# Kernel optimization log

Measured on AMD Instinct MI355X. Metric: run time of the kernel, lower is better.

## Reference

```python
import jax, jax.numpy as jnp
import numpy as np

KSIZE = 7
NSPIX = 196


def _unfold(x, k):
    # x: (T, C, H, W) -> (T, C, k*k, H, W), reflect padding, torch Unfold ordering
    p = (k - 1) // 2
    T, C, H, W = x.shape
    xp = jnp.pad(x, ((0, 0), (0, 0), (p, p), (p, p)), mode='reflect')
    return jnp.stack([xp[:, :, i:i + H, j:j + W] for i in range(k) for j in range(k)], axis=2)


def setup_inputs() -> dict:
    key = jax.random.key(0)
    k1, k2, k3, k4, k5 = jax.random.split(key, 5)
    T, C, H, W = 2, 64, 160, 160
    fan_in = C * KSIZE * KSIZE
    x = jax.random.normal(k1, (T, C, H, W), jnp.float32)
    spix = jax.random.randint(k2, (T, H, W), 0, NSPIX, jnp.int32)
    W_lin = jax.random.normal(k3, (C, fan_in), jnp.float32) / np.sqrt(fan_in)
    b_lin = jax.random.normal(k4, (C,), jnp.float32) * 0.01
    w_scale = jax.random.normal(k5, (C,), jnp.float32) / np.sqrt(C)
    b_scale = jnp.zeros((1,), jnp.float32)
    return {"x": x, "spix": spix, "W_lin": W_lin, "b_lin": b_lin,
            "w_scale": w_scale, "b_scale": b_scale}


def reference(x, spix, W_lin, b_lin, w_scale, b_scale):
    T, C, H, W = x.shape
    K2 = KSIZE * KSIZE
    O = W_lin.shape[0]
    p = (KSIZE - 1) // 2

    # unfold(x) with reflect padding -> patches (T, C, K2, H, W)
    patches = _unfold(x, KSIZE)

    # unfold(spix) -> neighbor superpixel ids per pixel (T, K2, H, W)
    sp = jnp.pad(spix, ((0, 0), (p, p), (p, p)), mode='reflect')
    nb = jnp.stack([sp[:, i:i + H, j:j + W] for i in range(KSIZE) for j in range(KSIZE)], axis=1)

    # per-frame superpixel mean pooling (bist.get_pooled_video): down (T, S, C)
    seg = (spix.astype(jnp.int32) + jnp.arange(T, dtype=jnp.int32)[:, None, None] * NSPIX).reshape(-1)
    feats = x.transpose(0, 2, 3, 1).reshape(-1, C)  # (T*H*W, C)
    sums = jax.ops.segment_sum(feats, seg, num_segments=T * NSPIX).reshape(T, NSPIX, C)
    cnts = jax.ops.segment_sum(jnp.ones((seg.shape[0],), x.dtype), seg,
                               num_segments=T * NSPIX).reshape(T, NSPIX, 1)
    down = sums / jnp.maximum(cnts, 1.0)

    # squared pairwise distances between superpixel means: pwd (T, S, S)
    sq = jnp.sum(down * down, axis=-1)
    pwd = jnp.maximum(sq[:, :, None] + sq[:, None, :]
                      - 2.0 * jnp.einsum('tsc,tuc->tsu', down, down), 0.0)

    # sims[t,k,h,w] = ||mean(spix[t,h,w]) - mean(nb[t,k,h,w])||^2
    tidx = jnp.arange(T)[:, None, None, None]
    sims = pwd[tidx, spix[:, None, :, :], nb]  # (T, K2, H, W)

    # scale = 10 * softplus(1x1-conv(x / ||x||_c))  -> (T, H, W)
    xn = x / (jnp.linalg.norm(x, axis=1, keepdims=True) + 1e-10)
    scale = 10.0 * jax.nn.softplus(jnp.einsum('c,tchw->thw', w_scale, xn) + b_scale[0])

    # apply_norm 'exp_max' over the kernel-tap axis
    rw = jnp.exp(-scale[:, None, :, :] * sims)  # (T, K2, H, W)
    rw = rw / (1e-5 + jnp.max(rw, axis=1, keepdims=True))

    # dynamic conv: out[t,o,h,w] = sum_{c,k} W[o,c,k] * patches[t,c,k,h,w] * rw[t,k,h,w] + b[o]
    out = jnp.einsum('ock,tckhw,tkhw->tohw', W_lin.reshape(O, C, K2), patches, rw)
    return out + b_lin[None, :, None, None]
```

## Files before the change

kernel.cpp:

```cpp
#include <hip/hip_runtime.h>
#include <math.h>

#define TT 2
#define CC 64
#define HH 160
#define WW 160
#define KS 7
#define K2 49
#define NSPIX 196
#define HWSZ (HH*WW)
#define PAD 3
#define OO 64
#define FANIN (CC*K2)
#define TS 8
#define PS (TS+KS-1)
#define NPOS (PS*PS)

#define NCHUNK 25
#define CHUNKPIX 1024

typedef _Float16 half8 __attribute__((ext_vector_type(8)));
typedef float f32x16 __attribute__((ext_vector_type(16)));
typedef unsigned int uint4v __attribute__((ext_vector_type(4)));
typedef _Float16 half2v __attribute__((ext_vector_type(2)));

__device__ __forceinline__ int reflect(int i, int n) {
    if (i < 0) i = -i;
    if (i >= n) i = 2*n - 2 - i;
    return i;
}

__global__ __launch_bounds__(256) void k_prep(const float* __restrict__ x,
                                              const int* __restrict__ spix,
                                              const float* __restrict__ Wl,
                                              const float* __restrict__ wsc,
                                              const float* __restrict__ bsc,
                                              float* __restrict__ sums,
                                              float* __restrict__ cnts,
                                              float* __restrict__ scale,
                                              _Float16* __restrict__ Wb,
                                              _Float16* __restrict__ xT) {
    __shared__ float ls[8*200];
    __shared__ float lcnt[200];
    int bid = blockIdx.x;
    int tid = threadIdx.x;

    if (bid < 400) {
        int cg = bid & 7;
        int rest = bid >> 3;
        int ch = rest % NCHUNK;
        int t  = rest / NCHUNK;

        for (int i = tid; i < 8*200; i += 256) ls[i] = 0.f;
        if (cg == 0) for (int i = tid; i < 200; i += 256) lcnt[i] = 0.f;
        __syncthreads();

        int base = ch*CHUNKPIX;
        const float* xb = x + ((size_t)t*CC + cg*8)*HWSZ;
        #pragma unroll
        for (int i = 0; i < CHUNKPIX; i += 256) {
            int pix = base + i + tid;
            int s = spix[t*HWSZ + pix];
            if (cg == 0) atomicAdd(&lcnt[s], 1.0f);
            #pragma unroll
            for (int j = 0; j < 8; ++j) atomicAdd(&ls[j*200 + s], xb[(size_t)j*HWSZ + pix]);
        }
        __syncthreads();

        float* sb = sums + (size_t)t*NSPIX*CC + cg*8;
        for (int i = tid; i < 8*NSPIX; i += 256) {
            int s = i >> 3, j = i & 7;
            float v = ls[j*200 + s];
            if (v != 0.f) atomicAdd(&sb[s*CC + j], v);
        }
        if (cg == 0)
            for (int i = tid; i < NSPIX; i += 256) {
                float v = lcnt[i];
                if (v != 0.f) atomicAdd(&cnts[t*NSPIX + i], v);
            }
    } else if (bid < 600) {
        int pix = (bid - 400)*256 + tid;
        int t = pix / HWSZ, hw = pix - t*HWSZ;
        const float* xs = x + (size_t)t*CC*HWSZ + hw;
        float s1 = 0.f, s2 = 0.f;
        unsigned int pk[32];
        #pragma unroll
        for (int cp = 0; cp < 32; ++cp) {
            float v0 = xs[(size_t)(2*cp)*HWSZ];
            float v1 = xs[(size_t)(2*cp + 1)*HWSZ];
            s1 += wsc[2*cp]*v0 + wsc[2*cp+1]*v1;
            s2 = fmaf(v0, v0, s2); s2 = fmaf(v1, v1, s2);
            half2v h; h[0] = (_Float16)v0; h[1] = (_Float16)v1;
            pk[cp] = __builtin_bit_cast(unsigned int, h);
        }
        float z = s1/(sqrtf(s2) + 1e-10f) + bsc[0];
        float sp_ = (z > 0.f) ? z + log1pf(expf(-z)) : log1pf(expf(z));
        scale[pix] = 10.f*sp_;
        uint4v* dst = (uint4v*)(xT + (size_t)pix*64);
        #pragma unroll
        for (int q = 0; q < 8; ++q) {
            uint4v v = { pk[4*q], pk[4*q+1], pk[4*q+2], pk[4*q+3] };
            dst[q] = v;
        }
    } else {
        int row = (bid - 600)*256 + tid;
        if (row < 2*K2*4*64) {
            int ln  = row & 63;
            int kc  = (row >> 6) & 3;
            int tq  = row >> 8;
            int tap = tq % K2;
            int qo  = tq / K2;
            int o = qo*32 + (ln & 31);
            int cb = kc*16 + (ln >> 5)*8;
            _Float16* dst = Wb + (size_t)row*8;
            const float* src = Wl + (size_t)o*FANIN + tap;
            #pragma unroll
            for (int j = 0; j < 8; ++j) dst[j] = (_Float16)src[(size_t)(cb + j)*K2];
        }
    }
}

__global__ __launch_bounds__(256) void k_pwd(const float* __restrict__ sums,
                                             const float* __restrict__ cnts,
                                             float* __restrict__ pwd) {
    int tid = blockIdx.x*256 + threadIdx.x;
    if (tid >= TT*NSPIX*NSPIX) return;
    int t = tid / (NSPIX*NSPIX); int r = tid - t*NSPIX*NSPIX;
    int s = r / NSPIX, u = r - (r / NSPIX)*NSPIX;
    const float* ds = sums + (size_t)(t*NSPIX + s)*CC;
    const float* du = sums + (size_t)(t*NSPIX + u)*CC;
    float is = 1.0f / fmaxf(cnts[t*NSPIX + s], 1.0f);
    float iu = 1.0f / fmaxf(cnts[t*NSPIX + u], 1.0f);
    float acc = 0.f;
    #pragma unroll 8
    for (int c = 0; c < CC; ++c) {
        float d = ds[c]*is - du[c]*iu;
        acc = fmaf(d, d, acc);
    }
    pwd[tid] = acc;
}

__device__ __forceinline__ void stageA(const _Float16* __restrict__ Wb,
                                       _Float16* dstbuf, int tap, int w, int ln) {
    const _Float16* g0 = Wb + (size_t)tap*2048 + (w*64 + ln)*8;
    const _Float16* g1 = g0 + (size_t)K2*2048;
    _Float16* l0 = dstbuf + w*512;
    _Float16* l1 = dstbuf + 2048 + w*512;
    __builtin_amdgcn_global_load_lds((const __attribute__((address_space(1))) unsigned int*)g0,
                                     (__attribute__((address_space(3))) unsigned int*)l0, 16, 0, 0);
    __builtin_amdgcn_global_load_lds((const __attribute__((address_space(1))) unsigned int*)g1,
                                     (__attribute__((address_space(3))) unsigned int*)l1, 16, 0, 0);
}

__global__ __launch_bounds__(256, 3) void k_main(
    const _Float16* __restrict__ xT, const int* __restrict__ spix,
    const _Float16* __restrict__ Wb, const float* __restrict__ b_lin,
    const float* __restrict__ pwd, const float* __restrict__ scale,
    float* __restrict__ out)
{
    __shared__ unsigned short xpT[NPOS*64];
    __shared__ unsigned short rwb[K2*64];
    __shared__ _Float16 Ast[2][4096];
    __shared__ int   sp[NPOS];
    __shared__ float mxp[4*64];

    int bid = blockIdx.x;
    int t = bid / 400;
    int r = bid - t*400;
    int th0 = (r / 20)*TS, tw0 = (r - (r/20)*20)*TS;
    int tid = threadIdx.y*64 + threadIdx.x;

    for (int i = tid; i < NPOS; i += 256) {
        int rr = reflect(th0 + i/PS - PAD, HH);
        int cc = reflect(tw0 + i%PS - PAD, WW);
        sp[i] = spix[t*HWSZ + rr*WW + cc];
    }
    {
        const _Float16* xt = xT + (size_t)t*HWSZ*64;
        for (int i = tid; i < NPOS*8; i += 256) {
            int pos = i >> 3, cb = i & 7;
            int rr = reflect(th0 + pos/PS - PAD, HH);
            int cc = reflect(tw0 + pos%PS - PAD, WW);
            uint4v v = *(const uint4v*)(xt + (size_t)(rr*WW + cc)*64 + cb*8);
            int chunk = cb ^ (pos & 7);
            *(uint4v*)&xpT[pos*64 + chunk*8] = v;
        }
    }
    __syncthreads();

    int ln = threadIdx.x;
    int wv = __builtin_amdgcn_readfirstlane(threadIdx.y);

    int p_ = threadIdx.x;
    int ty = threadIdx.y;
    int py0 = p_ >> 3, px0 = p_ & 7;
    {
        float sc = scale[t*HWSZ + (th0 + py0)*WW + (tw0 + px0)];
        int s0 = sp[(py0 + PAD)*PS + (px0 + PAD)];
        const float* pr = pwd + (t*NSPIX + s0)*NSPIX;
        float pmax = 0.f;
        for (int k = ty; k < K2; k += 4) {
            int di = k/KS, dj = k - di*KS;
            int nb = sp[(py0 + di)*PS + (px0 + dj)];
            float v = __expf(-sc * pr[nb]);
            rwb[k*64 + p_] = __builtin_bit_cast(unsigned short, (_Float16)v);
            pmax = fmaxf(pmax, v);
        }
        mxp[ty*64 + p_] = pmax;
    }
    stageA(Wb, &Ast[0][0], 0, wv, ln);
    __syncthreads();

    int qp = wv & 1, kh = wv >> 1;
    int p  = qp*32 + (ln & 31);
    int ppy = p >> 3, ppx = p & 7;
    int lhi = ln >> 5;

    int jc0 = 4*kh + lhi, jc1 = jc0 + 2;
    int aoff = 2*kh*512 + ln*8;

    f32x16 acc0, acc1;
    #pragma unroll
    for (int i = 0; i < 16; ++i) { acc0[i] = 0.f; acc1[i] = 0.f; }

    int buf = 0;
    int di = 0, dj = 0;
    for (int tap = 0; tap < K2; ++tap) {
        if (tap + 1 < K2) stageA(Wb, &Ast[buf ^ 1][0], tap + 1, wv, ln);

        const _Float16* ab = &Ast[buf][aoff];
        half8 A00 = *(const half8*)(ab);
        half8 A01 = *(const half8*)(ab + 512);
        half8 A10 = *(const half8*)(ab + 2048);
        half8 A11 = *(const half8*)(ab + 2048 + 512);

        int pos = (ppy + di)*PS + (ppx + dj);
        int sw  = pos & 7;
        const unsigned short* bbase = &xpT[pos*64];
        half8 B0 = *(const half8*)(bbase + ((jc0 ^ sw) << 3));
        half8 B1 = *(const half8*)(bbase + ((jc1 ^ sw) << 3));

        _Float16 rh = __builtin_bit_cast(_Float16, rwb[tap*64 + p]);
        half8 rv8 = { rh, rh, rh, rh, rh, rh, rh, rh };
        half8 b0 = B0 * rv8;
        half8 b1 = B1 * rv8;

        acc0 = __builtin_amdgcn_mfma_f32_32x32x16_f16(A00, b0, acc0, 0, 0, 0);
        acc1 = __builtin_amdgcn_mfma_f32_32x32x16_f16(A10, b0, acc1, 0, 0, 0);
        acc0 = __builtin_amdgcn_mfma_f32_32x32x16_f16(A01, b1, acc0, 0, 0, 0);
        acc1 = __builtin_amdgcn_mfma_f32_32x32x16_f16(A11, b1, acc1, 0, 0, 0);

        if (++dj == KS) { dj = 0; ++di; }
        __syncthreads();
        buf ^= 1;
    }

    float* red = (float*)xpT;
    if (kh == 1) {
        #pragma unroll
        for (int i = 0; i < 16; ++i) {
            red[((qp*2 + 0)*16 + i)*64 + ln] = acc0[i];
            red[((qp*2 + 1)*16 + i)*64 + ln] = acc1[i];
        }
    }
    __syncthreads();
    if (kh == 0) {
        float m = fmaxf(fmaxf(mxp[p], mxp[64 + p]), fmaxf(mxp[128 + p], mxp[192 + p]));
        float s = 1.f/(1e-5f + m);
        int h = th0 + ppy, w = tw0 + ppx;
        int row_hi = 4*lhi;
        float* ob = out + (size_t)t*OO*HWSZ + h*WW + w;
        #pragma unroll
        for (int rg = 0; rg < 16; ++rg) {
            int o0 = (rg & 3) + 8*(rg >> 2) + row_hi;
            int o1 = 32 + o0;
            float v0 = acc0[rg] + red[((qp*2 + 0)*16 + rg)*64 + ln];
            float v1 = acc1[rg] + red[((qp*2 + 1)*16 + rg)*64 + ln];
            ob[(size_t)o0*HWSZ] = v0*s + b_lin[o0];
            ob[(size_t)o1*HWSZ] = v1*s + b_lin[o1];
        }
    }
}

extern "C" void kernel_launch(void* const* d_in, const int* in_sizes, int n_in,
                              void* d_out, int out_size, void* d_ws, size_t ws_size,
                              hipStream_t stream) {
    const float* x    = (const float*)d_in[0];
    const int*   spix = (const int*)d_in[1];
    const float* Wl   = (const float*)d_in[2];
    const float* bl   = (const float*)d_in[3];
    const float* wsc  = (const float*)d_in[4];
    const float* bsc  = (const float*)d_in[5];
    float* out = (float*)d_out;

    float* ws    = (float*)d_ws;
    float* sums  = ws;
    float* cnts  = sums + TT*NSPIX*CC;
    float* pwd   = cnts + TT*NSPIX;
    float* scale = pwd  + TT*NSPIX*NSPIX;
    _Float16* Wb = (_Float16*)(scale + TT*HWSZ);
    _Float16* xT = Wb + (size_t)2*K2*4*64*8;

    hipMemsetAsync(sums, 0, (size_t)(TT*NSPIX*CC + TT*NSPIX)*sizeof(float), stream);

    k_prep<<<698, 256, 0, stream>>>(x, spix, Wl, wsc, bsc, sums, cnts, scale, Wb, xT);
    k_pwd <<<(TT*NSPIX*NSPIX + 255)/256, 256, 0, stream>>>(sums, cnts, pwd);

    dim3 blk(64, 4, 1);
    k_main<<<TT*400, blk, 0, stream>>>(xT, spix, Wb, bl, pwd, scale, out);
}
```

Baseline: 174.8 us.

## Fuse prep, pwd and main kernels into one persistent kernel with grid barriers

Merges the three kernel launches into a single 800-block kernel that runs the prep phase, a software grid barrier, the pairwise-distance phase, another barrier, and the dynamic-conv MFMA phase. The goal is to remove launch gaps and inter-kernel drain. It also drops the LDS double-buffering of weight tiles in favour of direct global loads with no per-tap __syncthreads, which frees LDS so occupancy can rise to 4 blocks. The barriers rely on all 800 blocks being co-resident, so the kernel risks deadlock if they are not. Reading weights straight from global may raise load latency in the inner loop.

```diff
diff --git a/kernel.cpp b/kernel.cpp
--- a/kernel.cpp
+++ b/kernel.cpp
@@ -18,6 +18,7 @@
 
 #define NCHUNK 25
 #define CHUNKPIX 1024
+#define NBLK 800
 
 typedef _Float16 half8 __attribute__((ext_vector_type(8)));
 typedef float f32x16 __attribute__((ext_vector_type(16)));
@@ -30,50 +31,73 @@
     return i;
 }
 
-__global__ __launch_bounds__(256) void k_prep(const float* __restrict__ x,
-                                              const int* __restrict__ spix,
-                                              const float* __restrict__ Wl,
-                                              const float* __restrict__ wsc,
-                                              const float* __restrict__ bsc,
-                                              float* __restrict__ sums,
-                                              float* __restrict__ cnts,
-                                              float* __restrict__ scale,
-                                              _Float16* __restrict__ Wb,
-                                              _Float16* __restrict__ xT) {
-    __shared__ float ls[8*200];
-    __shared__ float lcnt[200];
+__device__ __forceinline__ void grid_barrier(unsigned int* cnt, unsigned int* flag) {
+    __syncthreads();
+    if (threadIdx.x == 0 && threadIdx.y == 0) {
+        __threadfence();
+        unsigned int a = __hip_atomic_fetch_add(cnt, 1u, __ATOMIC_ACQ_REL,
+                                                __HIP_MEMORY_SCOPE_AGENT);
+        if (a == NBLK - 1u) {
+            __hip_atomic_store(flag, 1u, __ATOMIC_RELEASE, __HIP_MEMORY_SCOPE_AGENT);
+        } else {
+            while (__hip_atomic_load(flag, __ATOMIC_ACQUIRE,
+                                     __HIP_MEMORY_SCOPE_AGENT) == 0u)
+                __builtin_amdgcn_s_sleep(8);
+        }
+        __threadfence();
+    }
+    __syncthreads();
+}
+
+__global__ __launch_bounds__(256, 4) void k_fused(
+    const float* __restrict__ x, const int* __restrict__ spix,
+    const float* __restrict__ Wl, const float* __restrict__ b_lin,
+    const float* __restrict__ wsc, const float* __restrict__ bsc,
+    float* __restrict__ sums, float* __restrict__ cnts,
+    unsigned int* __restrict__ bar,
+    float* __restrict__ pwd, float* __restrict__ scale,
+    _Float16* __restrict__ Wb, _Float16* __restrict__ xT,
+    float* __restrict__ out)
+{
+    __shared__ unsigned short xpT[NPOS*64];
+    __shared__ unsigned short rwb[K2*64];
+    __shared__ int   sp[NPOS];
+    __shared__ float mxp[4*64];
+
     int bid = blockIdx.x;
-    int tid = threadIdx.x;
+    int tid = threadIdx.y*64 + threadIdx.x;
 
     if (bid < 400) {
-        int cg = bid & 7;
+        float* ls   = (float*)xpT;
+        float* lcnt = (float*)rwb;
+        int cg_ = bid & 7;
         int rest = bid >> 3;
         int ch = rest % NCHUNK;
         int t  = rest / NCHUNK;
 
         for (int i = tid; i < 8*200; i += 256) ls[i] = 0.f;
-        if (cg == 0) for (int i = tid; i < 200; i += 256) lcnt[i] = 0.f;
+        if (cg_ == 0) for (int i = tid; i < 200; i += 256) lcnt[i] = 0.f;
         __syncthreads();
 
         int base = ch*CHUNKPIX;
-        const float* xb = x + ((size_t)t*CC + cg*8)*HWSZ;
+        const float* xb = x + ((size_t)t*CC + cg_*8)*HWSZ;
         #pragma unroll
         for (int i = 0; i < CHUNKPIX; i += 256) {
             int pix = base + i + tid;
             int s = spix[t*HWSZ + pix];
-            if (cg == 0) atomicAdd(&lcnt[s], 1.0f);
+            if (cg_ == 0) atomicAdd(&lcnt[s], 1.0f);
             #pragma unroll
             for (int j = 0; j < 8; ++j) atomicAdd(&ls[j*200 + s], xb[(size_t)j*HWSZ + pix]);
         }
         __syncthreads();
 
-        float* sb = sums + (size_t)t*NSPIX*CC + cg*8;
+        float* sb = sums + (size_t)t*NSPIX*CC + cg_*8;
         for (int i = tid; i < 8*NSPIX; i += 256) {
             int s = i >> 3, j = i & 7;
             float v = ls[j*200 + s];
             if (v != 0.f) atomicAdd(&sb[s*CC + j], v);
         }
-        if (cg == 0)
+        if (cg_ == 0)
             for (int i = tid; i < NSPIX; i += 256) {
                 float v = lcnt[i];
                 if (v != 0.f) atomicAdd(&cnts[t*NSPIX + i], v);
@@ -102,7 +126,7 @@
             uint4v v = { pk[4*q], pk[4*q+1], pk[4*q+2], pk[4*q+3] };
             dst[q] = v;
         }
-    } else {
+    } else if (bid < 698) {
         int row = (bid - 600)*256 + tid;
         if (row < 2*K2*4*64) {
             int ln  = row & 63;
@@ -118,57 +142,40 @@
             for (int j = 0; j < 8; ++j) dst[j] = (_Float16)src[(size_t)(cb + j)*K2];
         }
     }
-}
-
-__global__ __launch_bounds__(256) void k_pwd(const float* __restrict__ sums,
-                                             const float* __restrict__ cnts,
-                                             float* __restrict__ pwd) {
-    int tid = blockIdx.x*256 + threadIdx.x;
-    if (tid >= TT*NSPIX*NSPIX) return;
-    int t = tid / (NSPIX*NSPIX); int r = tid - t*NSPIX*NSPIX;
-    int s = r / NSPIX, u = r - (r / NSPIX)*NSPIX;
-    const float* ds = sums + (size_t)(t*NSPIX + s)*CC;
-    const float* du = sums + (size_t)(t*NSPIX + u)*CC;
-    float is = 1.0f / fmaxf(cnts[t*NSPIX + s], 1.0f);
-    float iu = 1.0f / fmaxf(cnts[t*NSPIX + u], 1.0f);
-    float acc = 0.f;
-    #pragma unroll 8
-    for (int c = 0; c < CC; ++c) {
-        float d = ds[c]*is - du[c]*iu;
-        acc = fmaf(d, d, acc);
-    }
-    pwd[tid] = acc;
-}
-
-__device__ __forceinline__ void stageA(const _Float16* __restrict__ Wb,
-                                       _Float16* dstbuf, int tap, int w, int ln) {
-    const _Float16* g0 = Wb + (size_t)tap*2048 + (w*64 + ln)*8;
-    const _Float16* g1 = g0 + (size_t)K2*2048;
-    _Float16* l0 = dstbuf + w*512;
-    _Float16* l1 = dstbuf + 2048 + w*512;
-    __builtin_amdgcn_global_load_lds((const __attribute__((address_space(1))) unsigned int*)g0,
-                                     (__attribute__((address_space(3))) unsigned int*)l0, 16, 0, 0);
-    __builtin_amdgcn_global_load_lds((const __attribute__((address_space(1))) unsigned int*)g1,
-                                     (__attribute__((address_space(3))) unsigned int*)l1, 16, 0, 0);
-}
-
-__global__ __launch_bounds__(256, 3) void k_main(
-    const _Float16* __restrict__ xT, const int* __restrict__ spix,
-    const _Float16* __restrict__ Wb, const float* __restrict__ b_lin,
-    const float* __restrict__ pwd, const float* __restrict__ scale,
-    float* __restrict__ out)
-{
-    __shared__ unsigned short xpT[NPOS*64];
-    __shared__ unsigned short rwb[K2*64];
-    __shared__ _Float16 Ast[2][4096];
-    __shared__ int   sp[NPOS];
-    __shared__ float mxp[4*64];
-
-    int bid = blockIdx.x;
+
+    grid_barrier(&bar[0], &bar[1]);
+
+    {
+        int idx = bid*256 + tid;
+        if (idx < TT*NSPIX*NSPIX) {
+            int t = idx / (NSPIX*NSPIX); int r = idx - t*NSPIX*NSPIX;
+            int s = r / NSPIX, u = r - (r / NSPIX)*NSPIX;
+            const float4* ds4 = (const float4*)(sums + (size_t)(t*NSPIX + s)*CC);
+            const float4* du4 = (const float4*)(sums + (size_t)(t*NSPIX + u)*CC);
+            float is = 1.0f / fmaxf(cnts[t*NSPIX + s], 1.0f);
+            float iu = 1.0f / fmaxf(cnts[t*NSPIX + u], 1.0f);
+            float acc = 0.f;
+            #pragma unroll
+            for (int q = 0; q < 16; ++q) {
+                float4 a = ds4[q], b = du4[q];
+                float d0 = a.x*is - b.x*iu;
+                float d1 = a.y*is - b.y*iu;
+                float d2 = a.z*is - b.z*iu;
+                float d3 = a.w*is - b.w*iu;
+                acc = fmaf(d0, d0, acc);
+                acc = fmaf(d1, d1, acc);
+                acc = fmaf(d2, d2, acc);
+                acc = fmaf(d3, d3, acc);
+            }
+            pwd[idx] = acc;
+        }
+    }
+
+    grid_barrier(&bar[2], &bar[3]);
+
     int t = bid / 400;
     int r = bid - t*400;
     int th0 = (r / 20)*TS, tw0 = (r - (r/20)*20)*TS;
-    int tid = threadIdx.y*64 + threadIdx.x;
 
     for (int i = tid; i < NPOS; i += 256) {
         int rr = reflect(th0 + i/PS - PAD, HH);
@@ -187,9 +194,6 @@
         }
     }
     __syncthreads();
-
-    int ln = threadIdx.x;
-    int wv = __builtin_amdgcn_readfirstlane(threadIdx.y);
 
     int p_ = threadIdx.x;
     int ty = threadIdx.y;
@@ -208,31 +212,33 @@
         }
         mxp[ty*64 + p_] = pmax;
     }
-    stageA(Wb, &Ast[0][0], 0, wv, ln);
-    __syncthreads();
-
+    __syncthreads();
+
+    int ln = threadIdx.x;
+    int wv = __builtin_amdgcn_readfirstlane(threadIdx.y);
     int qp = wv & 1, kh = wv >> 1;
     int p  = qp*32 + (ln & 31);
     int ppy = p >> 3, ppx = p & 7;
     int lhi = ln >> 5;
 
     int jc0 = 4*kh + lhi, jc1 = jc0 + 2;
-    int aoff = 2*kh*512 + ln*8;
+
+    const _Float16* A0b = Wb + (size_t)(2*kh)*512 + ln*8;
+    const _Float16* A1b = A0b + (size_t)K2*4*512;
 
     f32x16 acc0, acc1;
     #pragma unroll
     for (int i = 0; i < 16; ++i) { acc0[i] = 0.f; acc1[i] = 0.f; }
 
-    int buf = 0;
     int di = 0, dj = 0;
+    #pragma unroll 7
     for (int tap = 0; tap < K2; ++tap) {
-        if (tap + 1 < K2) stageA(Wb, &Ast[buf ^ 1][0], tap + 1, wv, ln);
-
-        const _Float16* ab = &Ast[buf][aoff];
-        half8 A00 = *(const half8*)(ab);
-        half8 A01 = *(const half8*)(ab + 512);
-        half8 A10 = *(const half8*)(ab + 2048);
-        half8 A11 = *(const half8*)(ab + 2048 + 512);
+        const _Float16* a0 = A0b + (size_t)tap*2048;
+        half8 A00 = *(const half8*)(a0);
+        half8 A01 = *(const half8*)(a0 + 512);
+        const _Float16* a1 = A1b + (size_t)tap*2048;
+        half8 A10 = *(const half8*)(a1);
+        half8 A11 = *(const half8*)(a1 + 512);
 
         int pos = (ppy + di)*PS + (ppx + dj);
         int sw  = pos & 7;
@@ -251,10 +257,9 @@
         acc1 = __builtin_amdgcn_mfma_f32_32x32x16_f16(A11, b1, acc1, 0, 0, 0);
 
         if (++dj == KS) { dj = 0; ++di; }
-        __syncthreads();
-        buf ^= 1;
-    }
-
+    }
+
+    __syncthreads();
     float* red = (float*)xpT;
     if (kh == 1) {
         #pragma unroll
@@ -296,16 +301,15 @@
     float* ws    = (float*)d_ws;
     float* sums  = ws;
     float* cnts  = sums + TT*NSPIX*CC;
-    float* pwd   = cnts + TT*NSPIX;
+    unsigned int* bar = (unsigned int*)(cnts + TT*NSPIX);
+    float* pwd   = (float*)(bar + 8);
     float* scale = pwd  + TT*NSPIX*NSPIX;
     _Float16* Wb = (_Float16*)(scale + TT*HWSZ);
     _Float16* xT = Wb + (size_t)2*K2*4*64*8;
 
-    hipMemsetAsync(sums, 0, (size_t)(TT*NSPIX*CC + TT*NSPIX)*sizeof(float), stream);
-
-    k_prep<<<698, 256, 0, stream>>>(x, spix, Wl, wsc, bsc, sums, cnts, scale, Wb, xT);
-    k_pwd <<<(TT*NSPIX*NSPIX + 255)/256, 256, 0, stream>>>(sums, cnts, pwd);
-
-    dim3 blk(64, 4, 1);
-    k_main<<<TT*400, blk, 0, stream>>>(xT, spix, Wb, bl, pwd, scale, out);
+    hipMemsetAsync(sums, 0, (size_t)(TT*NSPIX*CC + TT*NSPIX + 8)*sizeof(float), stream);
+
+    k_fused<<<NBLK, dim3(64, 4, 1), 0, stream>>>(x, spix, Wl, bl, wsc, bsc,
+                                                 sums, cnts, bar, pwd, scale,
+                                                 Wb, xT, out);
 }
```

Result: slower. 466.4 us (+166.8%).

## Load weights directly from global in main loop, vectorize pooling and pwd

Applied to the files above, without the earlier changes.

The main conv kernel no longer double-buffers weight tiles through LDS with a barrier per tap. Each wave now reads its A fragments straight from global memory (L2-resident), which removes 49 block barriers and frees LDS so occupancy can rise to 4 blocks per CU; block IDs are also remapped to interleave tiles. The pooling kernel reads spix and x as int4/float4 and merges atomic adds when adjacent pixels share a superpixel, and the pairwise-distance kernel uses float4 loads. The risk is higher global/L2 latency in the MFMA loop with no explicit prefetch.

```diff
diff --git a/kernel.cpp b/kernel.cpp
--- a/kernel.cpp
+++ b/kernel.cpp
@@ -56,14 +56,29 @@
         __syncthreads();
 
         int base = ch*CHUNKPIX;
-        const float* xb = x + ((size_t)t*CC + cg*8)*HWSZ;
-        #pragma unroll
-        for (int i = 0; i < CHUNKPIX; i += 256) {
-            int pix = base + i + tid;
-            int s = spix[t*HWSZ + pix];
-            if (cg == 0) atomicAdd(&lcnt[s], 1.0f);
-            #pragma unroll
-            for (int j = 0; j < 8; ++j) atomicAdd(&ls[j*200 + s], xb[(size_t)j*HWSZ + pix]);
+        const int4* sp4 = (const int4*)(spix + t*HWSZ + base);
+        int4 sv = sp4[tid];
+        bool uni = (sv.x == sv.y) && (sv.y == sv.z) && (sv.z == sv.w);
+        if (cg == 0) {
+            if (uni) atomicAdd(&lcnt[sv.x], 4.0f);
+            else {
+                atomicAdd(&lcnt[sv.x], 1.f); atomicAdd(&lcnt[sv.y], 1.f);
+                atomicAdd(&lcnt[sv.z], 1.f); atomicAdd(&lcnt[sv.w], 1.f);
+            }
+        }
+        const float* xb = x + ((size_t)t*CC + cg*8)*HWSZ + base;
+        #pragma unroll
+        for (int j = 0; j < 8; ++j) {
+            float4 xv = *(const float4*)(xb + (size_t)j*HWSZ + tid*4);
+            float* lj = &ls[j*200];
+            if (uni) {
+                atomicAdd(&lj[sv.x], xv.x + xv.y + xv.z + xv.w);
+            } else {
+                if (sv.x == sv.y) atomicAdd(&lj[sv.x], xv.x + xv.y);
+                else { atomicAdd(&lj[sv.x], xv.x); atomicAdd(&lj[sv.y], xv.y); }
+                if (sv.z == sv.w) atomicAdd(&lj[sv.z], xv.z + xv.w);
+                else { atomicAdd(&lj[sv.z], xv.z); atomicAdd(&lj[sv.w], xv.w); }
+            }
         }
         __syncthreads();
 
@@ -127,32 +142,27 @@
     if (tid >= TT*NSPIX*NSPIX) return;
     int t = tid / (NSPIX*NSPIX); int r = tid - t*NSPIX*NSPIX;
     int s = r / NSPIX, u = r - (r / NSPIX)*NSPIX;
-    const float* ds = sums + (size_t)(t*NSPIX + s)*CC;
-    const float* du = sums + (size_t)(t*NSPIX + u)*CC;
+    const float4* ds4 = (const float4*)(sums + (size_t)(t*NSPIX + s)*CC);
+    const float4* du4 = (const float4*)(sums + (size_t)(t*NSPIX + u)*CC);
     float is = 1.0f / fmaxf(cnts[t*NSPIX + s], 1.0f);
     float iu = 1.0f / fmaxf(cnts[t*NSPIX + u], 1.0f);
     float acc = 0.f;
-    #pragma unroll 8
-    for (int c = 0; c < CC; ++c) {
-        float d = ds[c]*is - du[c]*iu;
-        acc = fmaf(d, d, acc);
+    #pragma unroll
+    for (int q = 0; q < 16; ++q) {
+        float4 a = ds4[q], b = du4[q];
+        float d0 = a.x*is - b.x*iu;
+        float d1 = a.y*is - b.y*iu;
+        float d2 = a.z*is - b.z*iu;
+        float d3 = a.w*is - b.w*iu;
+        acc = fmaf(d0, d0, acc);
+        acc = fmaf(d1, d1, acc);
+        acc = fmaf(d2, d2, acc);
+        acc = fmaf(d3, d3, acc);
     }
     pwd[tid] = acc;
 }
 
-__device__ __forceinline__ void stageA(const _Float16* __restrict__ Wb,
-                                       _Float16* dstbuf, int tap, int w, int ln) {
-    const _Float16* g0 = Wb + (size_t)tap*2048 + (w*64 + ln)*8;
-    const _Float16* g1 = g0 + (size_t)K2*2048;
-    _Float16* l0 = dstbuf + w*512;
-    _Float16* l1 = dstbuf + 2048 + w*512;
-    __builtin_amdgcn_global_load_lds((const __attribute__((address_space(1))) unsigned int*)g0,
-                                     (__attribute__((address_space(3))) unsigned int*)l0, 16, 0, 0);
-    __builtin_amdgcn_global_load_lds((const __attribute__((address_space(1))) unsigned int*)g1,
-                                     (__attribute__((address_space(3))) unsigned int*)l1, 16, 0, 0);
-}
-
-__global__ __launch_bounds__(256, 3) void k_main(
+__global__ __launch_bounds__(256, 4) void k_main(
     const _Float16* __restrict__ xT, const int* __restrict__ spix,
     const _Float16* __restrict__ Wb, const float* __restrict__ b_lin,
     const float* __restrict__ pwd, const float* __restrict__ scale,
@@ -160,11 +170,11 @@
 {
     __shared__ unsigned short xpT[NPOS*64];
     __shared__ unsigned short rwb[K2*64];
-    __shared__ _Float16 Ast[2][4096];
     __shared__ int   sp[NPOS];
     __shared__ float mxp[4*64];
 
-    int bid = blockIdx.x;
+    int bid0 = blockIdx.x;
+    int bid = (bid0 & 7)*100 + (bid0 >> 3);
     int t = bid / 400;
     int r = bid - t*400;
     int th0 = (r / 20)*TS, tw0 = (r - (r/20)*20)*TS;
@@ -187,9 +197,6 @@
         }
     }
     __syncthreads();
-
-    int ln = threadIdx.x;
-    int wv = __builtin_amdgcn_readfirstlane(threadIdx.y);
 
     int p_ = threadIdx.x;
     int ty = threadIdx.y;
@@ -208,31 +215,33 @@
         }
         mxp[ty*64 + p_] = pmax;
     }
-    stageA(Wb, &Ast[0][0], 0, wv, ln);
     __syncthreads();
 
+    int ln = threadIdx.x;
+    int wv = __builtin_amdgcn_readfirstlane(threadIdx.y);
     int qp = wv & 1, kh = wv >> 1;
     int p  = qp*32 + (ln & 31);
     int ppy = p >> 3, ppx = p & 7;
     int lhi = ln >> 5;
 
     int jc0 = 4*kh + lhi, jc1 = jc0 + 2;
-    int aoff = 2*kh*512 + ln*8;
+
+    const _Float16* A0b = Wb + (size_t)(2*kh)*512 + ln*8;
+    const _Float16* A1b = A0b + (size_t)K2*4*512;
 
     f32x16 acc0, acc1;
     #pragma unroll
     for (int i = 0; i < 16; ++i) { acc0[i] = 0.f; acc1[i] = 0.f; }
 
-    int buf = 0;
     int di = 0, dj = 0;
+    #pragma unroll 7
     for (int tap = 0; tap < K2; ++tap) {
-        if (tap + 1 < K2) stageA(Wb, &Ast[buf ^ 1][0], tap + 1, wv, ln);
-
-        const _Float16* ab = &Ast[buf][aoff];
-        half8 A00 = *(const half8*)(ab);
-        half8 A01 = *(const half8*)(ab + 512);
-        half8 A10 = *(const half8*)(ab + 2048);
-        half8 A11 = *(const half8*)(ab + 2048 + 512);
+        const _Float16* a0 = A0b + (size_t)tap*2048;
+        half8 A00 = *(const half8*)(a0);
+        half8 A01 = *(const half8*)(a0 + 512);
+        const _Float16* a1 = A1b + (size_t)tap*2048;
+        half8 A10 = *(const half8*)(a1);
+        half8 A11 = *(const half8*)(a1 + 512);
 
         int pos = (ppy + di)*PS + (ppx + dj);
         int sw  = pos & 7;
@@ -251,10 +260,9 @@
         acc1 = __builtin_amdgcn_mfma_f32_32x32x16_f16(A11, b1, acc1, 0, 0, 0);
 
         if (++dj == KS) { dj = 0; ++di; }
-        __syncthreads();
-        buf ^= 1;
-    }
-
+    }
+
+    __syncthreads();
     float* red = (float*)xpT;
     if (kh == 1) {
         #pragma unroll
```

After: 148.8 us. 1.17x faster.
